# Kernel optimization log

Measured on AMD Instinct MI355X. Metric: run time of the kernel, lower is better.

The kernel has to match this reference:

```python
import jax, jax.numpy as jnp
import numpy as np

W_CHAMFER = 1.0
W_SMOOTH = 0.5
K_NEIGHBORS = 8


def _pairwise_sqdist(a, b):
    # a: [B,N,3], b: [B,M,3] -> [B,N,M] squared euclidean distances
    a2 = jnp.sum(a * a, axis=-1)  # [B,N]
    b2 = jnp.sum(b * b, axis=-1)  # [B,M]
    ab = jnp.einsum('bnd,bmd->bnm', a, b)  # [B,N,M]
    d2 = a2[:, :, None] + b2[:, None, :] - 2.0 * ab
    return jnp.maximum(d2, 0.0)


def _chamfer(pc1, pc2):
    d = jnp.sqrt(_pairwise_sqdist(pc1, pc2))  # [B,N,M] euclidean (matches torch.norm)
    d1 = jnp.min(d, axis=2)  # [B,N]
    d2 = jnp.min(d, axis=1)  # [B,M]
    return jnp.mean(d1) + jnp.mean(d2)


def _smoothness(pc, flow, k=K_NEIGHBORS):
    d2 = _pairwise_sqdist(pc, pc)  # [B,N,N]
    # k+1 nearest (squared dist preserves ordering); drop self (index 0)
    _, idx = jax.lax.top_k(-d2, k + 1)  # [B,N,k+1]
    idx = idx[:, :, 1:]  # [B,N,k]
    neighbor_flow = jax.vmap(lambda f, i: f[i])(flow, idx)  # [B,N,k,3]
    diff = flow[:, :, None, :] - neighbor_flow
    return jnp.mean(jnp.linalg.norm(diff, axis=-1))


def setup_inputs() -> dict:
    key = jax.random.key(0)
    k1, k2, k3 = jax.random.split(key, 3)
    B, N, M = 2, 8192, 8192
    pc1 = jax.random.normal(k1, (B, N, 3), dtype=jnp.float32)
    pc2 = jax.random.normal(k2, (B, M, 3), dtype=jnp.float32)
    pred_flow = jax.random.normal(k3, (B, N, 3), dtype=jnp.float32) * 0.1
    return {"pc1": pc1, "pc2": pc2, "pred_flow": pred_flow}


def reference(pc1, pc2, pred_flow):
    pc1_warped = pc1 + pred_flow
    l_chamfer = _chamfer(pc1_warped, pc2)
    l_smooth = _smoothness(pc1, pred_flow)
    return W_CHAMFER * l_chamfer + W_SMOOTH * l_smooth
```

## Files before the change

kernel.cpp:

```cpp
#include <hip/hip_runtime.h>

#define N_PTS 8192
#define BATCH 2
#define KNN 8
#define STILE 2048
#define PPB 16
#define CH_R 8
#define CH_SLICE 256

__device__ __forceinline__ void ce(unsigned &x, unsigned &y) {
    unsigned lo = min(x, y), hi = max(x, y); x = lo; y = hi;
}

__device__ __forceinline__ void insert4(unsigned o[4], unsigned key) {
    unsigned n0 = min(o[0], key);
    unsigned n1 = max(o[0], min(o[1], key));
    unsigned n2 = max(o[1], min(o[2], key));
    unsigned n3 = max(o[2], min(o[3], key));
    o[0]=n0; o[1]=n1; o[2]=n2; o[3]=n3;
}

__device__ __forceinline__ void merge_stage8(unsigned m[8], int d) {
    unsigned p[8], c[8];
    #pragma unroll
    for (int k = 0; k < 8; ++k) p[k] = __shfl_xor(m[k], d, 64);
    #pragma unroll
    for (int k = 0; k < 8; ++k) c[k] = min(m[k], p[7-k]);
    ce(c[0],c[4]); ce(c[1],c[5]); ce(c[2],c[6]); ce(c[3],c[7]);
    ce(c[0],c[2]); ce(c[1],c[3]); ce(c[4],c[6]); ce(c[5],c[7]);
    ce(c[0],c[1]); ce(c[2],c[3]); ce(c[4],c[5]); ce(c[6],c[7]);
    #pragma unroll
    for (int k = 0; k < 8; ++k) m[k] = c[k];
}

__device__ __forceinline__ void merge64(unsigned m[8]) {
    merge_stage8(m, 1); merge_stage8(m, 2); merge_stage8(m, 4);
    merge_stage8(m, 8); merge_stage8(m, 16); merge_stage8(m, 32);
}

__global__ void init_kernel(unsigned int* __restrict__ mins, float* __restrict__ out, int n) {
    int i = blockIdx.x * blockDim.x + threadIdx.x;
    if (i < n) mins[i] = 0x7F800000u;
    if (i == 0) out[0] = 0.0f;
}

__global__ __launch_bounds__(256, 4) void chamfer_min_kernel(const float* __restrict__ pc1,
                                                             const float* __restrict__ pc2,
                                                             const float* __restrict__ flow,
                                                             unsigned* __restrict__ mins) {
    const int z = blockIdx.z;
    const int b = z & 1, dir = z >> 1;
    const int tid = threadIdx.x;
    const float* base1 = pc1 + (size_t)b * N_PTS * 3;
    const float* base2 = pc2 + (size_t)b * N_PTS * 3;
    const float* fl    = flow + (size_t)b * N_PTS * 3;

    __shared__ float  sraw[CH_SLICE * 3];
    __shared__ float4 sq[CH_SLICE];
    const int m0 = blockIdx.y * CH_SLICE;

    if (tid < CH_SLICE * 3 / 4) {
        float4 v;
        if (dir == 0) {
            v = ((const float4*)(base2 + (size_t)m0 * 3))[tid];
        } else {
            float4 a = ((const float4*)(base1 + (size_t)m0 * 3))[tid];
            float4 f = ((const float4*)(fl    + (size_t)m0 * 3))[tid];
            v = make_float4(a.x + f.x, a.y + f.y, a.z + f.z, a.w + f.w);
        }
        ((float4*)sraw)[tid] = v;
    }

    const int i0 = blockIdx.x * (256 * CH_R) + tid * CH_R;
    float mx[CH_R], my_[CH_R], mz_[CH_R], p2[CH_R], best[CH_R];
    #pragma unroll
    for (int r = 0; r < CH_R; ++r) {
        int row = i0 + r;
        float px, py, pz;
        if (dir == 0) {
            px = base1[row*3+0] + fl[row*3+0];
            py = base1[row*3+1] + fl[row*3+1];
            pz = base1[row*3+2] + fl[row*3+2];
        } else {
            px = base2[row*3+0]; py = base2[row*3+1]; pz = base2[row*3+2];
        }
        mx[r] = -2.0f * px; my_[r] = -2.0f * py; mz_[r] = -2.0f * pz;
        p2[r] = fmaf(px, px, fmaf(py, py, pz * pz));
        best[r] = __builtin_inff();
    }
    __syncthreads();
    {
        float qx = sraw[tid*3+0], qy = sraw[tid*3+1], qz = sraw[tid*3+2];
        sq[tid] = make_float4(qx, qy, qz, fmaf(qx, qx, fmaf(qy, qy, qz * qz)));
    }
    __syncthreads();

    #pragma unroll 1
    for (int g = 0; g < CH_SLICE; g += 8) {
        float4 q[8];
        #pragma unroll
        for (int u = 0; u < 8; ++u) q[u] = sq[g + u];
        #pragma unroll
        for (int u = 0; u < 8; ++u) {
            #pragma unroll
            for (int r = 0; r < CH_R; ++r) {
                float s = fmaf(mx[r], q[u].x, fmaf(my_[r], q[u].y, fmaf(mz_[r], q[u].z, q[u].w)));
                best[r] = fminf(best[r], s);
            }
        }
    }
    #pragma unroll
    for (int r = 0; r < CH_R; ++r) {
        float d2 = fmaxf(best[r] + p2[r], 0.0f);
        atomicMin(&mins[((size_t)dir * BATCH + b) * N_PTS + i0 + r], __float_as_uint(d2));
    }
}

__global__ void chamfer_reduce_kernel(const unsigned int* __restrict__ mins,
                                      float* __restrict__ out) {
    int i = blockIdx.x * 256 + threadIdx.x;
    float v = sqrtf(__uint_as_float(mins[i])) * (1.0f / (float)(BATCH * N_PTS));
    #pragma unroll
    for (int off = 32; off > 0; off >>= 1) v += __shfl_down(v, off, 64);
    __shared__ float wsum[4];
    int wid = threadIdx.x >> 6;
    if ((threadIdx.x & 63) == 0) wsum[wid] = v;
    __syncthreads();
    if (threadIdx.x == 0) {
        atomicAdd(out, wsum[0] + wsum[1] + wsum[2] + wsum[3]);
    }
}

__global__ __launch_bounds__(256, 4) void smooth_kernel(const float* __restrict__ pc1,
                                                        const float* __restrict__ flow,
                                                        float* __restrict__ out) {
    const int b = blockIdx.y;
    const int tid = threadIdx.x;
    const int wv = tid >> 6, lane = tid & 63;
    const int i0w = blockIdx.x * PPB + wv * 4;
    const float* P = pc1  + (size_t)b * N_PTS * 3;
    const float* F = flow + (size_t)b * N_PTS * 3;

    float mx[4], my[4], mz[4], p2[4], gr[4];
    #pragma unroll
    for (int r = 0; r < 4; ++r) {
        int i = i0w + r;
        float px = P[i*3+0], py = P[i*3+1], pz = P[i*3+2];
        mx[r] = -2.0f * px; my[r] = -2.0f * py; mz[r] = -2.0f * pz;
        p2[r] = fmaf(px, px, fmaf(py, py, pz * pz));
        gr[r] = __builtin_inff();
    }

    unsigned o[4][4];
    #pragma unroll
    for (int r = 0; r < 4; ++r) {
        #pragma unroll
        for (int k = 0; k < 4; ++k) o[r][k] = 0xFFFFFFFFu;
    }

    __shared__ float4 sq[STILE];
    __shared__ float psum[4];

    #pragma unroll 1
    for (int tile = 0; tile < N_PTS / STILE; ++tile) {
        const int t0 = tile * STILE;
        __syncthreads();
        for (int u = tid; u < STILE; u += 256) {
            int g = t0 + u;
            float qx = P[g*3+0], qy = P[g*3+1], qz = P[g*3+2];
            sq[u] = make_float4(qx, qy, qz, fmaf(qx, qx, fmaf(qy, qy, qz * qz)));
        }
        __syncthreads();

        if (tile == 0) {
            float4 qa = sq[lane];
            #pragma unroll 1
            for (int st = 0; st < 32; ++st) {
                float4 qb = sq[(((st + 1) & 31) * 64) + lane];
                int j = st * 64 + lane;
                #pragma unroll
                for (int r = 0; r < 4; ++r) {
                    float s = fmaf(mx[r], qa.x, fmaf(my[r], qa.y, fmaf(mz[r], qa.z, qa.w)));
                    float d2 = fmaxf(s + p2[r], 0.0f);
                    unsigned key = (__float_as_uint(d2) & 0xFFFFE000u) | (unsigned)j;
                    key = (j == i0w + r) ? 0xFFFFFFFFu : key;
                    insert4(o[r], key);
                }
                qa = qb;
            }
            #pragma unroll
            for (int r = 0; r < 4; ++r) {
                unsigned m[8] = {o[r][0], o[r][1], o[r][2], o[r][3],
                                 0xFFFFFFFFu, 0xFFFFFFFFu, 0xFFFFFFFFu, 0xFFFFFFFFu};
                merge64(m);
                float thr_up = __uint_as_float((m[7] & 0xFFFFE000u) + 0x4000u);
                gr[r] = thr_up - p2[r];
            }
        } else {
            float4 qa = sq[lane];
            #pragma unroll 1
            for (int st = 0; st < 32; ++st) {
                float4 qb = sq[(((st + 1) & 31) * 64) + lane];
                int j = t0 + st * 64 + lane;
                float s0 = fmaf(mx[0], qa.x, fmaf(my[0], qa.y, fmaf(mz[0], qa.z, qa.w)));
                float s1 = fmaf(mx[1], qa.x, fmaf(my[1], qa.y, fmaf(mz[1], qa.z, qa.w)));
                float s2 = fmaf(mx[2], qa.x, fmaf(my[2], qa.y, fmaf(mz[2], qa.z, qa.w)));
                float s3 = fmaf(mx[3], qa.x, fmaf(my[3], qa.y, fmaf(mz[3], qa.z, qa.w)));
                if (__any(s0 <= gr[0])) {
                    float d2 = fmaxf(s0 + p2[0], 0.0f);
                    unsigned key = (__float_as_uint(d2) & 0xFFFFE000u) | (unsigned)j;
                    key = (j == i0w + 0) ? 0xFFFFFFFFu : key;
                    insert4(o[0], key);
                }
                if (__any(s1 <= gr[1])) {
                    float d2 = fmaxf(s1 + p2[1], 0.0f);
                    unsigned key = (__float_as_uint(d2) & 0xFFFFE000u) | (unsigned)j;
                    key = (j == i0w + 1) ? 0xFFFFFFFFu : key;
                    insert4(o[1], key);
                }
                if (__any(s2 <= gr[2])) {
                    float d2 = fmaxf(s2 + p2[2], 0.0f);
                    unsigned key = (__float_as_uint(d2) & 0xFFFFE000u) | (unsigned)j;
                    key = (j == i0w + 2) ? 0xFFFFFFFFu : key;
                    insert4(o[2], key);
                }
                if (__any(s3 <= gr[3])) {
                    float d2 = fmaxf(s3 + p2[3], 0.0f);
                    unsigned key = (__float_as_uint(d2) & 0xFFFFE000u) | (unsigned)j;
                    key = (j == i0w + 3) ? 0xFFFFFFFFu : key;
                    insert4(o[3], key);
                }
                qa = qb;
            }
        }
    }

    unsigned fin[4][8];
    #pragma unroll
    for (int r = 0; r < 4; ++r) {
        unsigned m[8] = {o[r][0], o[r][1], o[r][2], o[r][3],
                         0xFFFFFFFFu, 0xFFFFFFFFu, 0xFFFFFFFFu, 0xFFFFFFFFu};
        merge64(m);
        #pragma unroll
        for (int k = 0; k < 8; ++k) fin[r][k] = m[k];
    }

    const int sel = lane & 31;
    unsigned key = fin[0][0];
    #pragma unroll
    for (int rr = 0; rr < 4; ++rr) {
        #pragma unroll
        for (int kk = 0; kk < 8; ++kk) {
            if (sel == rr * 8 + kk) key = fin[rr][kk];
        }
    }
    const int r = sel >> 3;
    const int i = i0w + r;
    const int j = (int)(key & (N_PTS - 1));
    float dx = F[i*3+0] - F[j*3+0];
    float dy = F[i*3+1] - F[j*3+1];
    float dz = F[i*3+2] - F[j*3+2];
    float s = sqrtf(fmaf(dx, dx, fmaf(dy, dy, dz * dz)));
    #pragma unroll
    for (int d = 1; d < 64; d <<= 1) s += __shfl_xor(s, d, 64);
    if (lane == 0) psum[wv] = s;
    __syncthreads();
    if (tid == 0) {
        atomicAdd(out, (psum[0] + psum[1] + psum[2] + psum[3]) *
                       (0.25f / ((float)BATCH * N_PTS * KNN)));
    }
}

extern "C" void kernel_launch(void* const* d_in, const int* in_sizes, int n_in,
                              void* d_out, int out_size, void* d_ws, size_t ws_size,
                              hipStream_t stream) {
    const float* pc1  = (const float*)d_in[0];
    const float* pc2  = (const float*)d_in[1];
    const float* flow = (const float*)d_in[2];
    float* out = (float*)d_out;
    unsigned int* mins = (unsigned int*)d_ws;

    init_kernel<<<dim3(128), 256, 0, stream>>>(mins, out, 2 * BATCH * N_PTS);

    dim3 gch(N_PTS / (256 * CH_R), N_PTS / CH_SLICE, 2 * BATCH);
    chamfer_min_kernel<<<gch, 256, 0, stream>>>(pc1, pc2, flow, mins);

    chamfer_reduce_kernel<<<dim3(2 * BATCH * N_PTS / 256), 256, 0, stream>>>(mins, out);

    smooth_kernel<<<dim3(N_PTS / PPB, BATCH), 256, 0, stream>>>(pc1, flow, out);
}
```

Measured before the change: 161.1 us.

## Precompute float4 point arrays, drop atomics for partial-min stores, retune chamfer and kNN threshold

Adds a prep kernel that packs warped pc1, pc2 and pc1 into float4 arrays with squared norms, so the chamfer and smoothness kernels read aligned float4 data instead of recomputing norms. The chamfer kernel now reads candidates straight from global memory with register prefetch instead of shared memory, uses 4 rows per thread, and can store per-slice partial mins for a separate reduction instead of using atomicMin. The smoothness kernel drops the per-candidate self-exclusion check in favour of a single post-pass removal, and updates its pruning threshold after each of the first three tiles using a cheap shuffle estimate instead of a full merge. The cost is extra launches, extra workspace traffic for the partial buffer, and a looser, approximate threshold estimate.

```diff
diff --git a/kernel.cpp b/kernel.cpp
--- a/kernel.cpp
+++ b/kernel.cpp
@@ -5,8 +5,17 @@
 #define KNN 8
 #define STILE 2048
 #define PPB 16
-#define CH_R 8
+#define CH_R 4
 #define CH_SLICE 256
+#define NSLICE (N_PTS / CH_SLICE)
+#define PF 8
+
+#define OFF_Q1W 0
+#define OFF_Q2  (256*1024)
+#define OFF_Q1  (512*1024)
+#define OFF_MINS (768*1024)
+#define OFF_PART (896*1024)
+#define WS_STORE_NEED  (896*1024 + 4*1024*1024)
 
 __device__ __forceinline__ void ce(unsigned &x, unsigned &y) {
     unsigned lo = min(x, y), hi = max(x, y); x = lo; y = hi;
@@ -38,125 +47,129 @@
     merge_stage8(m, 8); merge_stage8(m, 16); merge_stage8(m, 32);
 }
 
-__global__ void init_kernel(unsigned int* __restrict__ mins, float* __restrict__ out, int n) {
-    int i = blockIdx.x * blockDim.x + threadIdx.x;
-    if (i < n) mins[i] = 0x7F800000u;
-    if (i == 0) out[0] = 0.0f;
-}
-
-__global__ __launch_bounds__(256, 4) void chamfer_min_kernel(const float* __restrict__ pc1,
-                                                             const float* __restrict__ pc2,
-                                                             const float* __restrict__ flow,
-                                                             unsigned* __restrict__ mins) {
+__global__ void prep_kernel(const float* __restrict__ pc1, const float* __restrict__ pc2,
+                            const float* __restrict__ flow,
+                            float4* __restrict__ q1w, float4* __restrict__ q2f,
+                            float4* __restrict__ q1f, unsigned* __restrict__ mins,
+                            float* __restrict__ out, int init_mins) {
+    int idx = blockIdx.x * 256 + threadIdx.x;
+    if (idx == 0) out[0] = 0.0f;
+    if (init_mins) { mins[idx] = 0x7F800000u; mins[idx + 16384] = 0x7F800000u; }
+    float x1 = pc1[idx*3+0], y1 = pc1[idx*3+1], z1 = pc1[idx*3+2];
+    float fx = flow[idx*3+0], fy = flow[idx*3+1], fz = flow[idx*3+2];
+    float x2 = pc2[idx*3+0], y2 = pc2[idx*3+1], z2 = pc2[idx*3+2];
+    float wx = x1 + fx, wy = y1 + fy, wz = z1 + fz;
+    q1w[idx] = make_float4(wx, wy, wz, fmaf(wx, wx, fmaf(wy, wy, wz * wz)));
+    q2f[idx] = make_float4(x2, y2, z2, fmaf(x2, x2, fmaf(y2, y2, z2 * z2)));
+    q1f[idx] = make_float4(x1, y1, z1, fmaf(x1, x1, fmaf(y1, y1, z1 * z1)));
+}
+
+__global__ __launch_bounds__(256, 4) void chamfer_min_kernel(
+        const float4* __restrict__ q1w, const float4* __restrict__ q2f,
+        unsigned* __restrict__ mins, float* __restrict__ part, int store_mode) {
     const int z = blockIdx.z;
     const int b = z & 1, dir = z >> 1;
     const int tid = threadIdx.x;
-    const float* base1 = pc1 + (size_t)b * N_PTS * 3;
-    const float* base2 = pc2 + (size_t)b * N_PTS * 3;
-    const float* fl    = flow + (size_t)b * N_PTS * 3;
-
-    __shared__ float  sraw[CH_SLICE * 3];
-    __shared__ float4 sq[CH_SLICE];
+    const float4* rows  = (dir == 0 ? q1w : q2f) + b * N_PTS;
+    const float4* cands = (dir == 0 ? q2f : q1w) + b * N_PTS;
     const int m0 = blockIdx.y * CH_SLICE;
-
-    if (tid < CH_SLICE * 3 / 4) {
-        float4 v;
-        if (dir == 0) {
-            v = ((const float4*)(base2 + (size_t)m0 * 3))[tid];
-        } else {
-            float4 a = ((const float4*)(base1 + (size_t)m0 * 3))[tid];
-            float4 f = ((const float4*)(fl    + (size_t)m0 * 3))[tid];
-            v = make_float4(a.x + f.x, a.y + f.y, a.z + f.z, a.w + f.w);
-        }
-        ((float4*)sraw)[tid] = v;
-    }
-
     const int i0 = blockIdx.x * (256 * CH_R) + tid * CH_R;
+
     float mx[CH_R], my_[CH_R], mz_[CH_R], p2[CH_R], best[CH_R];
     #pragma unroll
     for (int r = 0; r < CH_R; ++r) {
-        int row = i0 + r;
-        float px, py, pz;
-        if (dir == 0) {
-            px = base1[row*3+0] + fl[row*3+0];
-            py = base1[row*3+1] + fl[row*3+1];
-            pz = base1[row*3+2] + fl[row*3+2];
-        } else {
-            px = base2[row*3+0]; py = base2[row*3+1]; pz = base2[row*3+2];
-        }
-        mx[r] = -2.0f * px; my_[r] = -2.0f * py; mz_[r] = -2.0f * pz;
-        p2[r] = fmaf(px, px, fmaf(py, py, pz * pz));
+        float4 p = rows[i0 + r];
+        mx[r] = -2.0f * p.x; my_[r] = -2.0f * p.y; mz_[r] = -2.0f * p.z;
+        p2[r] = p.w;
         best[r] = __builtin_inff();
     }
-    __syncthreads();
-    {
-        float qx = sraw[tid*3+0], qy = sraw[tid*3+1], qz = sraw[tid*3+2];
-        sq[tid] = make_float4(qx, qy, qz, fmaf(qx, qx, fmaf(qy, qy, qz * qz)));
-    }
-    __syncthreads();
-
+
+    const float4* Qc = cands + m0;
+    float4 q[PF];
+    #pragma unroll
+    for (int u = 0; u < PF; ++u) q[u] = Qc[u];
     #pragma unroll 1
-    for (int g = 0; g < CH_SLICE; g += 8) {
-        float4 q[8];
-        #pragma unroll
-        for (int u = 0; u < 8; ++u) q[u] = sq[g + u];
-        #pragma unroll
-        for (int u = 0; u < 8; ++u) {
+    for (int g = 0; g < CH_SLICE; g += PF) {
+        float4 qn[PF];
+        const int nb = (g + PF < CH_SLICE) ? g + PF : 0;
+        #pragma unroll
+        for (int u = 0; u < PF; ++u) qn[u] = Qc[nb + u];
+        #pragma unroll
+        for (int u = 0; u < PF; ++u) {
             #pragma unroll
             for (int r = 0; r < CH_R; ++r) {
                 float s = fmaf(mx[r], q[u].x, fmaf(my_[r], q[u].y, fmaf(mz_[r], q[u].z, q[u].w)));
                 best[r] = fminf(best[r], s);
             }
         }
-    }
-    #pragma unroll
-    for (int r = 0; r < CH_R; ++r) {
-        float d2 = fmaxf(best[r] + p2[r], 0.0f);
-        atomicMin(&mins[((size_t)dir * BATCH + b) * N_PTS + i0 + r], __float_as_uint(d2));
-    }
-}
-
-__global__ void chamfer_reduce_kernel(const unsigned int* __restrict__ mins,
-                                      float* __restrict__ out) {
-    int i = blockIdx.x * 256 + threadIdx.x;
-    float v = sqrtf(__uint_as_float(mins[i])) * (1.0f / (float)(BATCH * N_PTS));
-    #pragma unroll
-    for (int off = 32; off > 0; off >>= 1) v += __shfl_down(v, off, 64);
+        #pragma unroll
+        for (int u = 0; u < PF; ++u) q[u] = qn[u];
+    }
+
+    if (store_mode) {
+        float4 v;
+        v.x = fmaxf(best[0] + p2[0], 0.0f);
+        v.y = fmaxf(best[1] + p2[1], 0.0f);
+        v.z = fmaxf(best[2] + p2[2], 0.0f);
+        v.w = fmaxf(best[3] + p2[3], 0.0f);
+        *(float4*)(part + ((size_t)(z * NSLICE + blockIdx.y)) * N_PTS + i0) = v;
+    } else {
+        #pragma unroll
+        for (int r = 0; r < CH_R; ++r) {
+            float d2 = fmaxf(best[r] + p2[r], 0.0f);
+            atomicMin(&mins[z * N_PTS + i0 + r], __float_as_uint(d2));
+        }
+    }
+}
+
+__global__ void chamfer_reduce_kernel(const unsigned* __restrict__ mins,
+                                      const float* __restrict__ part,
+                                      float* __restrict__ out, int store_mode) {
+    int t = blockIdx.x * 256 + threadIdx.x;
+    float v;
+    if (store_mode) {
+        int c = t >> 13, row = t & (N_PTS - 1);
+        const float* p = part + ((size_t)c * NSLICE) * N_PTS + row;
+        v = __builtin_inff();
+        #pragma unroll 8
+        for (int s = 0; s < NSLICE; ++s) v = fminf(v, p[(size_t)s * N_PTS]);
+    } else {
+        v = __uint_as_float(mins[t]);
+    }
+    float d = sqrtf(v) * (1.0f / (float)(BATCH * N_PTS));
+    #pragma unroll
+    for (int off = 32; off > 0; off >>= 1) d += __shfl_down(d, off, 64);
     __shared__ float wsum[4];
     int wid = threadIdx.x >> 6;
-    if ((threadIdx.x & 63) == 0) wsum[wid] = v;
+    if ((threadIdx.x & 63) == 0) wsum[wid] = d;
     __syncthreads();
-    if (threadIdx.x == 0) {
-        atomicAdd(out, wsum[0] + wsum[1] + wsum[2] + wsum[3]);
-    }
-}
-
-__global__ __launch_bounds__(256, 4) void smooth_kernel(const float* __restrict__ pc1,
+    if (threadIdx.x == 0) atomicAdd(out, wsum[0] + wsum[1] + wsum[2] + wsum[3]);
+}
+
+__global__ __launch_bounds__(256, 4) void smooth_kernel(const float4* __restrict__ q1f,
                                                         const float* __restrict__ flow,
                                                         float* __restrict__ out) {
     const int b = blockIdx.y;
     const int tid = threadIdx.x;
     const int wv = tid >> 6, lane = tid & 63;
     const int i0w = blockIdx.x * PPB + wv * 4;
-    const float* P = pc1  + (size_t)b * N_PTS * 3;
-    const float* F = flow + (size_t)b * N_PTS * 3;
+    const float4* Q = q1f + b * N_PTS;
+    const float*  F = flow + (size_t)b * N_PTS * 3;
 
     float mx[4], my[4], mz[4], p2[4], gr[4];
     #pragma unroll
     for (int r = 0; r < 4; ++r) {
-        int i = i0w + r;
-        float px = P[i*3+0], py = P[i*3+1], pz = P[i*3+2];
-        mx[r] = -2.0f * px; my[r] = -2.0f * py; mz[r] = -2.0f * pz;
-        p2[r] = fmaf(px, px, fmaf(py, py, pz * pz));
+        float4 p = Q[i0w + r];
+        mx[r] = -2.0f * p.x; my[r] = -2.0f * p.y; mz[r] = -2.0f * p.z;
+        p2[r] = p.w;
         gr[r] = __builtin_inff();
     }
 
     unsigned o[4][4];
     #pragma unroll
-    for (int r = 0; r < 4; ++r) {
+    for (int r = 0; r < 4; ++r)
         #pragma unroll
         for (int k = 0; k < 4; ++k) o[r][k] = 0xFFFFFFFFu;
-    }
 
     __shared__ float4 sq[STILE];
     __shared__ float psum[4];
@@ -165,17 +178,14 @@
     for (int tile = 0; tile < N_PTS / STILE; ++tile) {
         const int t0 = tile * STILE;
         __syncthreads();
-        for (int u = tid; u < STILE; u += 256) {
-            int g = t0 + u;
-            float qx = P[g*3+0], qy = P[g*3+1], qz = P[g*3+2];
-            sq[u] = make_float4(qx, qy, qz, fmaf(qx, qx, fmaf(qy, qy, qz * qz)));
-        }
+        #pragma unroll
+        for (int u = tid; u < STILE; u += 256) sq[u] = Q[t0 + u];
         __syncthreads();
 
         if (tile == 0) {
             float4 qa = sq[lane];
             #pragma unroll 1
-            for (int st = 0; st < 32; ++st) {
+            for (int st = 0; st < STILE / 64; ++st) {
                 float4 qb = sq[(((st + 1) & 31) * 64) + lane];
                 int j = st * 64 + lane;
                 #pragma unroll
@@ -183,23 +193,14 @@
                     float s = fmaf(mx[r], qa.x, fmaf(my[r], qa.y, fmaf(mz[r], qa.z, qa.w)));
                     float d2 = fmaxf(s + p2[r], 0.0f);
                     unsigned key = (__float_as_uint(d2) & 0xFFFFE000u) | (unsigned)j;
-                    key = (j == i0w + r) ? 0xFFFFFFFFu : key;
                     insert4(o[r], key);
                 }
                 qa = qb;
-            }
-            #pragma unroll
-            for (int r = 0; r < 4; ++r) {
-                unsigned m[8] = {o[r][0], o[r][1], o[r][2], o[r][3],
-                                 0xFFFFFFFFu, 0xFFFFFFFFu, 0xFFFFFFFFu, 0xFFFFFFFFu};
-                merge64(m);
-                float thr_up = __uint_as_float((m[7] & 0xFFFFE000u) + 0x4000u);
-                gr[r] = thr_up - p2[r];
             }
         } else {
             float4 qa = sq[lane];
             #pragma unroll 1
-            for (int st = 0; st < 32; ++st) {
+            for (int st = 0; st < STILE / 64; ++st) {
                 float4 qb = sq[(((st + 1) & 31) * 64) + lane];
                 int j = t0 + st * 64 + lane;
                 float s0 = fmaf(mx[0], qa.x, fmaf(my[0], qa.y, fmaf(mz[0], qa.z, qa.w)));
@@ -208,31 +209,50 @@
                 float s3 = fmaf(mx[3], qa.x, fmaf(my[3], qa.y, fmaf(mz[3], qa.z, qa.w)));
                 if (__any(s0 <= gr[0])) {
                     float d2 = fmaxf(s0 + p2[0], 0.0f);
-                    unsigned key = (__float_as_uint(d2) & 0xFFFFE000u) | (unsigned)j;
-                    key = (j == i0w + 0) ? 0xFFFFFFFFu : key;
-                    insert4(o[0], key);
+                    insert4(o[0], (__float_as_uint(d2) & 0xFFFFE000u) | (unsigned)j);
                 }
                 if (__any(s1 <= gr[1])) {
                     float d2 = fmaxf(s1 + p2[1], 0.0f);
-                    unsigned key = (__float_as_uint(d2) & 0xFFFFE000u) | (unsigned)j;
-                    key = (j == i0w + 1) ? 0xFFFFFFFFu : key;
-                    insert4(o[1], key);
+                    insert4(o[1], (__float_as_uint(d2) & 0xFFFFE000u) | (unsigned)j);
                 }
                 if (__any(s2 <= gr[2])) {
                     float d2 = fmaxf(s2 + p2[2], 0.0f);
-                    unsigned key = (__float_as_uint(d2) & 0xFFFFE000u) | (unsigned)j;
-                    key = (j == i0w + 2) ? 0xFFFFFFFFu : key;
-                    insert4(o[2], key);
+                    insert4(o[2], (__float_as_uint(d2) & 0xFFFFE000u) | (unsigned)j);
                 }
                 if (__any(s3 <= gr[3])) {
                     float d2 = fmaxf(s3 + p2[3], 0.0f);
-                    unsigned key = (__float_as_uint(d2) & 0xFFFFE000u) | (unsigned)j;
-                    key = (j == i0w + 3) ? 0xFFFFFFFFu : key;
-                    insert4(o[3], key);
+                    insert4(o[3], (__float_as_uint(d2) & 0xFFFFE000u) | (unsigned)j);
                 }
                 qa = qb;
             }
         }
+
+        if (tile <= 2) {
+            #pragma unroll
+            for (int r = 0; r < 4; ++r) {
+                unsigned a = max(o[r][2], (unsigned)__shfl_xor((int)o[r][2], 1, 64));
+                a = max(a, (unsigned)__shfl_xor((int)a, 2, 64));
+                a = min(a, (unsigned)__shfl_xor((int)a, 4, 64));
+                a = min(a, (unsigned)__shfl_xor((int)a, 8, 64));
+                a = min(a, (unsigned)__shfl_xor((int)a, 16, 64));
+                a = min(a, (unsigned)__shfl_xor((int)a, 32, 64));
+                float thr_up = __uint_as_float((a & 0xFFFFE000u) + 0x4000u);
+                gr[r] = thr_up - p2[r];
+            }
+        }
+    }
+
+    #pragma unroll
+    for (int r = 0; r < 4; ++r) {
+        const unsigned ii = (unsigned)(i0w + r);
+        bool m0 = (o[r][0] & 8191u) == ii;
+        bool m1 = m0 | ((o[r][1] & 8191u) == ii);
+        bool m2 = m1 | ((o[r][2] & 8191u) == ii);
+        bool m3 = m2 | ((o[r][3] & 8191u) == ii);
+        o[r][0] = m0 ? o[r][1] : o[r][0];
+        o[r][1] = m1 ? o[r][2] : o[r][1];
+        o[r][2] = m2 ? o[r][3] : o[r][2];
+        o[r][3] = m3 ? 0xFFFFFFFFu : o[r][3];
     }
 
     unsigned fin[4][8];
@@ -248,12 +268,10 @@
     const int sel = lane & 31;
     unsigned key = fin[0][0];
     #pragma unroll
-    for (int rr = 0; rr < 4; ++rr) {
-        #pragma unroll
-        for (int kk = 0; kk < 8; ++kk) {
+    for (int rr = 0; rr < 4; ++rr)
+        #pragma unroll
+        for (int kk = 0; kk < 8; ++kk)
             if (sel == rr * 8 + kk) key = fin[rr][kk];
-        }
-    }
     const int r = sel >> 3;
     const int i = i0w + r;
     const int j = (int)(key & (N_PTS - 1));
@@ -278,14 +296,23 @@
     const float* pc2  = (const float*)d_in[1];
     const float* flow = (const float*)d_in[2];
     float* out = (float*)d_out;
-    unsigned int* mins = (unsigned int*)d_ws;
-
-    init_kernel<<<dim3(128), 256, 0, stream>>>(mins, out, 2 * BATCH * N_PTS);
-
-    dim3 gch(N_PTS / (256 * CH_R), N_PTS / CH_SLICE, 2 * BATCH);
-    chamfer_min_kernel<<<gch, 256, 0, stream>>>(pc1, pc2, flow, mins);
-
-    chamfer_reduce_kernel<<<dim3(2 * BATCH * N_PTS / 256), 256, 0, stream>>>(mins, out);
-
-    smooth_kernel<<<dim3(N_PTS / PPB, BATCH), 256, 0, stream>>>(pc1, flow, out);
-}
+    char* ws = (char*)d_ws;
+
+    float4* q1w  = (float4*)(ws + OFF_Q1W);
+    float4* q2f  = (float4*)(ws + OFF_Q2);
+    float4* q1f  = (float4*)(ws + OFF_Q1);
+    unsigned* mins = (unsigned*)(ws + OFF_MINS);
+    float* part  = (float*)(ws + OFF_PART);
+
+    const int store_mode = (ws_size >= (size_t)WS_STORE_NEED) ? 1 : 0;
+
+    prep_kernel<<<dim3(16384 / 256), 256, 0, stream>>>(pc1, pc2, flow, q1w, q2f, q1f,
+                                                       mins, out, store_mode ? 0 : 1);
+
+    dim3 gch(N_PTS / (256 * CH_R), NSLICE, 2 * BATCH);
+    chamfer_min_kernel<<<gch, 256, 0, stream>>>(q1w, q2f, mins, part, store_mode);
+
+    chamfer_reduce_kernel<<<dim3(2 * BATCH * N_PTS / 256), 256, 0, stream>>>(mins, part, out, store_mode);
+
+    smooth_kernel<<<dim3(N_PTS / PPB, BATCH), 256, 0, stream>>>(q1f, flow, out);
+}
```

Measured after the change: 165.1 us. 1.02x slower.
